# Performance work log

Hardware: AMD Instinct MI355X
Metric: run time of the kernel (lower is better)

Reference implementation:

```python
import jax, jax.numpy as jnp
import numpy as np

N, E, F, K = 50000, 320000, 256, 2

def setup_inputs() -> dict:
    key = jax.random.key(0)
    k0, k1, k2, k3 = jax.random.split(key, 4)
    x = jax.random.normal(k0, (N, F), dtype=jnp.float32)
    edge_index = jax.random.randint(k1, (2, E), 0, N, dtype=jnp.int64)
    s = 1.0 / np.sqrt(F)
    init_weight = jax.random.uniform(k2, (K, F, F), jnp.float32, -s, s)
    root_weight = jax.random.uniform(k3, (K, F, F), jnp.float32, -s, s)
    bias = jnp.zeros((K, 1, F), dtype=jnp.float32)
    return {"x": x, "edge_index": edge_index, "init_weight": init_weight,
            "root_weight": root_weight, "bias": bias}

def reference(x, edge_index, init_weight, root_weight, bias):
    src = edge_index[0]
    dst = edge_index[1]
    n = x.shape[0]
    # gcn_norm without self-loops: deg over target index, sym normalization
    deg = jax.ops.segment_sum(jnp.ones((E,), x.dtype), dst, num_segments=n)
    dinv = jnp.where(deg > 0, jax.lax.rsqrt(jnp.maximum(deg, 1.0)), 0.0)
    w = dinv[src] * dinv[dst]                                   # [E]
    # ARMAConv, num_layers=1: out = act(A_hat @ (x W_k) + x V_k + b_k), mean over K
    h = jnp.einsum('nf,kfg->kng', x, init_weight)               # [K,N,F]
    msg = h[:, src, :] * w[None, :, None]                       # [K,E,F]
    agg = jax.vmap(lambda m: jax.ops.segment_sum(m, dst, num_segments=n))(msg)  # [K,N,F]
    root = jnp.einsum('nf,kfg->kng', x, root_weight)            # [K,N,F]
    arma = jax.nn.relu(agg + root + bias).mean(axis=0)          # [N,F]
    return x + jax.nn.relu(arma)
```

## Files before the change

### kernel.cpp

```cpp
#include <hip/hip_runtime.h>

#define NN 50000
#define NE 320000
#define FF 256
#define FILL_B 1250
#define XCVT_B 12500
#define BPREP_B 128
#define PSTR 64

typedef short short8 __attribute__((ext_vector_type(8)));
typedef float f32x4 __attribute__((ext_vector_type(4)));
typedef unsigned short us4 __attribute__((ext_vector_type(4)));
typedef unsigned short us8 __attribute__((ext_vector_type(8)));

static __device__ __forceinline__ unsigned short f2bf(float f) {
    union { float f; unsigned u; } v; v.f = f;
    unsigned r = v.u + 0x7FFFu + ((v.u >> 16) & 1u);
    return (unsigned short)(r >> 16);
}
static __device__ __forceinline__ float bf2f(unsigned short h) {
    return __uint_as_float((unsigned)h << 16);
}

__global__ __launch_bounds__(256)
void k_pre(const int* __restrict__ ei, int* __restrict__ cnt, int* __restrict__ padded,
           const float* __restrict__ x, unsigned short* __restrict__ Ab,
           const float* __restrict__ wi, const float* __restrict__ wr,
           unsigned short* __restrict__ Bp) {
    const int b = blockIdx.x;
    if (b < FILL_B) {
        int e = b * 256 + threadIdx.x;
        if (e < NE) {
            int src = ei[e];
            int dst = ei[NE + e];
            int slot = atomicAdd(&cnt[dst], 1);
            if (slot < PSTR) padded[(size_t)dst * PSTR + slot] = src;
        }
    } else if (b < FILL_B + XCVT_B) {
        int t = (b - FILL_B) * 256 + threadIdx.x;
        if (t < NN * 64) {
            int n = t >> 6, q = t & 63;
            float4 v = *reinterpret_cast<const float4*>(&x[(size_t)n * FF + q * 4]);
            us4 o = {f2bf(v.x), f2bf(v.y), f2bf(v.z), f2bf(v.w)};
            char* rowp = (char*)(Ab + (size_t)n * 512);
            *reinterpret_cast<us4*>(rowp + ((512 + q * 8) ^ ((n & 7) << 4))) = o;
        }
    } else {
        int t = (b - FILL_B - XCVT_B) * 256 + threadIdx.x;
        int l = t & 63;
        int fb = t >> 6;
        int kc = fb >> 5;
        int cf = fb & 31;
        int col = cf * 16 + (l & 15);
        int kpart = col >> 8;
        int g = col & 255;
        int K0 = kc * 32 + (l >> 4) * 8;
        unsigned short* dst = Bp + (size_t)fb * 512 + (size_t)l * 8;
        #pragma unroll
        for (int e = 0; e < 8; ++e) {
            int K = K0 + e;
            const float* srcp = (K < 256) ? wi : wr;
            float v = srcp[(size_t)kpart * 65536 + (size_t)(K & 255) * 256 + g];
            dst[e] = f2bf(v);
        }
    }
}

__global__ __launch_bounds__(256)
void k_agg(const int* __restrict__ cnt, const int* __restrict__ padded,
           unsigned short* __restrict__ Ab) {
    int wid = (blockIdx.x * blockDim.x + threadIdx.x) >> 6;
    if (wid >= NN / 2) return;
    int l = threadIdx.x & 63;
    int n = wid * 2 + (l >> 5);
    int d = cnt[n];
    float di = d > 0 ? rsqrtf((float)d) : 0.f;
    if (d > PSTR) d = PSTR;
    const int* pp = padded + (size_t)n * PSTR;
    const char* base = (const char*)Ab;
    const int lq = (l & 31) * 16;
    const int lb = 512 + lq;
    float acc[8];
    #pragma unroll
    for (int j = 0; j < 8; ++j) acc[j] = 0.f;
    int e = 0;
    for (; e + 4 <= d; e += 4) {
        int s0 = pp[e + 0];
        int s1 = pp[e + 1];
        int s2 = pp[e + 2];
        int s3 = pp[e + 3];
        us8 v0 = *reinterpret_cast<const us8*>(base + (size_t)s0 * 1024 + (lb ^ ((s0 & 7) << 4)));
        us8 v1 = *reinterpret_cast<const us8*>(base + (size_t)s1 * 1024 + (lb ^ ((s1 & 7) << 4)));
        us8 v2 = *reinterpret_cast<const us8*>(base + (size_t)s2 * 1024 + (lb ^ ((s2 & 7) << 4)));
        us8 v3 = *reinterpret_cast<const us8*>(base + (size_t)s3 * 1024 + (lb ^ ((s3 & 7) << 4)));
        int c0 = cnt[s0], c1 = cnt[s1], c2 = cnt[s2], c3 = cnt[s3];
        float w0 = di * (c0 > 0 ? rsqrtf((float)c0) : 0.f);
        float w1 = di * (c1 > 0 ? rsqrtf((float)c1) : 0.f);
        float w2 = di * (c2 > 0 ? rsqrtf((float)c2) : 0.f);
        float w3 = di * (c3 > 0 ? rsqrtf((float)c3) : 0.f);
        #pragma unroll
        for (int j = 0; j < 8; ++j)
            acc[j] = fmaf(w0, bf2f(v0[j]), fmaf(w1, bf2f(v1[j]),
                     fmaf(w2, bf2f(v2[j]), fmaf(w3, bf2f(v3[j]), acc[j]))));
    }
    for (; e < d; ++e) {
        int s0 = pp[e];
        us8 v0 = *reinterpret_cast<const us8*>(base + (size_t)s0 * 1024 + (lb ^ ((s0 & 7) << 4)));
        int c0 = cnt[s0];
        float w0 = di * (c0 > 0 ? rsqrtf((float)c0) : 0.f);
        #pragma unroll
        for (int j = 0; j < 8; ++j)
            acc[j] = fmaf(w0, bf2f(v0[j]), acc[j]);
    }
    us8 o;
    #pragma unroll
    for (int j = 0; j < 8; ++j) o[j] = f2bf(acc[j]);
    *reinterpret_cast<us8*>((char*)Ab + (size_t)n * 1024 + (lq ^ ((n & 7) << 4))) = o;
}

#define LOADB(dst, kc_)                                                           \
    {                                                                             \
        dst[0] = *reinterpret_cast<const short8*>(bpb + (kc_) * 32768 + (2 * w + 0) * 1024);        \
        dst[1] = *reinterpret_cast<const short8*>(bpb + (kc_) * 32768 + (2 * w + 1) * 1024);        \
        dst[2] = *reinterpret_cast<const short8*>(bpb + (kc_) * 32768 + (16 + 2 * w) * 1024);       \
        dst[3] = *reinterpret_cast<const short8*>(bpb + (kc_) * 32768 + (17 + 2 * w) * 1024);       \
    }
#define LOADA1K(dst, ab, kc2_)                                                    \
    {                                                                             \
        _Pragma("unroll")                                                         \
        for (int rf = 0; rf < 4; ++rf)                                            \
            dst[rf] = *reinterpret_cast<const short8*>((ab) + rf * 16384 + (kc2_) * 128); \
    }
#define MFMA4(aset, bset)                                                         \
    {                                                                             \
        _Pragma("unroll")                                                         \
        for (int rf = 0; rf < 4; ++rf)                                            \
            _Pragma("unroll")                                                     \
            for (int c = 0; c < 4; ++c)                                           \
                acc[rf][c] = __builtin_amdgcn_mfma_f32_16x16x32_bf16(aset[rf], bset[c], acc[rf][c], 0, 0, 0); \
    }

__global__ __launch_bounds__(512, 4)
void k_mm(const unsigned short* __restrict__ Ab, const unsigned short* __restrict__ Bp,
          const float* __restrict__ bias, float* __restrict__ out) {
    __shared__ char smem[65536];

    const int l = threadIdx.x & 63;
    const int w = threadIdx.x >> 6;
    const int row0 = blockIdx.x * 64;

    {
        const char* base = (const char*)Ab;
        #pragma unroll
        for (int j = 0; j < 8; ++j) {
            int rl = j * 8 + w;
            int rsrc = row0 + rl; if (rsrc >= NN) rsrc = NN - 1;
            const char* gp = base + (size_t)rsrc * 1024 + l * 16;
            __builtin_amdgcn_global_load_lds(
                (const __attribute__((address_space(1))) void*)gp,
                (__attribute__((address_space(3))) void*)(smem + rl * 1024),
                16, 0, 0);
        }
    }
    __syncthreads();

    f32x4 acc[4][4];
    #pragma unroll
    for (int i = 0; i < 4; ++i)
        #pragma unroll
        for (int j = 0; j < 4; ++j) acc[i][j] = (f32x4){0.f, 0.f, 0.f, 0.f};

    const int p = l & 7, q = l >> 4;
    const char* abase0 = smem + (l & 15) * 1024 + ((p >> 2) << 6) + ((q ^ (p & 3)) << 4);
    const char* abase1 = smem + (((size_t)(abase0 - smem)) ^ 64);
    const char* bpb = (const char*)(Bp + (size_t)l * 8);

    short8 b0[4], b1[4], a[4];
    LOADB(b0, 0)
    #pragma unroll 1
    for (int kc2 = 0; kc2 < 7; ++kc2) {
        LOADA1K(a, abase0, kc2)
        LOADB(b1, 2 * kc2 + 1)
        MFMA4(a, b0)
        LOADA1K(a, abase1, kc2)
        LOADB(b0, 2 * kc2 + 2)
        MFMA4(a, b1)
    }
    {
        LOADA1K(a, abase0, 7)
        LOADB(b1, 15)
        MFMA4(a, b0)
        LOADA1K(a, abase1, 7)
        MFMA4(a, b1)
    }

    __syncthreads();

    #pragma unroll
    for (int rf = 0; rf < 4; ++rf) {
        const int rl0 = rf * 16 + (l >> 4) * 4;
        #pragma unroll
        for (int j = 0; j < 4; ++j) {
            int rl = rl0 + j;
            int r = row0 + rl;
            if (r >= NN) continue;
            int sw = (rl & 7) << 4;
            #pragma unroll
            for (int c = 0; c < 2; ++c) {
                int gg = w * 32 + c * 16 + (l & 15);
                unsigned short xb =
                    *reinterpret_cast<const unsigned short*>(&smem[rl * 1024 + ((512 + gg * 2) ^ sw)]);
                float xv = bf2f(xb);
                float c0 = acc[rf][c][j] + bias[gg];
                float c1 = acc[rf][c + 2][j] + bias[256 + gg];
                float arma = 0.5f * (fmaxf(c0, 0.f) + fmaxf(c1, 0.f));
                out[(size_t)r * FF + gg] = xv + fmaxf(arma, 0.f);
            }
        }
    }
}

extern "C" void kernel_launch(void* const* d_in, const int* in_sizes, int n_in,
                              void* d_out, int out_size, void* d_ws, size_t ws_size,
                              hipStream_t stream) {
    const float* x    = (const float*)d_in[0];
    const int*   ei   = (const int*)d_in[1];
    const float* wi   = (const float*)d_in[2];
    const float* wr   = (const float*)d_in[3];
    const float* bias = (const float*)d_in[4];
    float* out = (float*)d_out;

    int* cnt    = (int*)d_ws;
    int* padded = cnt + NN;
    unsigned short* Bp = (unsigned short*)(padded + (size_t)NN * PSTR);
    unsigned short* Ab = (unsigned short*)d_out;

    hipMemsetAsync(cnt, 0, NN * sizeof(int), stream);

    k_pre<<<FILL_B + XCVT_B + BPREP_B, 256, 0, stream>>>(ei, cnt, padded, x, Ab, wi, wr, Bp);
    k_agg<<<(NN / 2 * 64 + 255) / 256, 256, 0, stream>>>(cnt, padded, Ab);
    k_mm <<<(NN + 63) / 64, 512, 0, stream>>>(Ab, Bp, bias, out);
}
```

Measured before the change: 108.2 us.

## Split A tile into two K-halves in LDS and start MFMA after first half arrives

```diff
diff --git a/kernel.cpp b/kernel.cpp
--- a/kernel.cpp
+++ b/kernel.cpp
@@ -125,11 +125,11 @@
         dst[2] = *reinterpret_cast<const short8*>(bpb + (kc_) * 32768 + (16 + 2 * w) * 1024);       \
         dst[3] = *reinterpret_cast<const short8*>(bpb + (kc_) * 32768 + (17 + 2 * w) * 1024);       \
     }
-#define LOADA1K(dst, ab, kc2_)                                                    \
+#define LOADAF(dst, ab, h_)                                                       \
     {                                                                             \
         _Pragma("unroll")                                                         \
         for (int rf = 0; rf < 4; ++rf)                                            \
-            dst[rf] = *reinterpret_cast<const short8*>((ab) + rf * 16384 + (kc2_) * 128); \
+            dst[rf] = *reinterpret_cast<const short8*>((ab) + rf * 8192 + (h_) * 128); \
     }
 #define MFMA4(aset, bset)                                                         \
     {                                                                             \
@@ -148,21 +148,30 @@
     const int l = threadIdx.x & 63;
     const int w = threadIdx.x >> 6;
     const int row0 = blockIdx.x * 64;
-
-    {
-        const char* base = (const char*)Ab;
-        #pragma unroll
-        for (int j = 0; j < 8; ++j) {
-            int rl = j * 8 + w;
-            int rsrc = row0 + rl; if (rsrc >= NN) rsrc = NN - 1;
-            const char* gp = base + (size_t)rsrc * 1024 + l * 16;
-            __builtin_amdgcn_global_load_lds(
-                (const __attribute__((address_space(1))) void*)gp,
-                (__attribute__((address_space(3))) void*)(smem + rl * 1024),
-                16, 0, 0);
-        }
-    }
-    __syncthreads();
+    const char* base = (const char*)Ab;
+
+    #pragma unroll
+    for (int j = 0; j < 4; ++j) {
+        int rl = w * 8 + 2 * j;
+        int r = row0 + rl + (l >> 5);
+        if (r >= NN) r = NN - 1;
+        const char* gp = base + (size_t)r * 1024 + (l & 31) * 16;
+        __builtin_amdgcn_global_load_lds(
+            (const __attribute__((address_space(1))) void*)gp,
+            (__attribute__((address_space(3))) void*)(smem + rl * 512),
+            16, 0, 0);
+    }
+    #pragma unroll
+    for (int j = 0; j < 4; ++j) {
+        int rl = w * 8 + 2 * j;
+        int r = row0 + rl + (l >> 5);
+        if (r >= NN) r = NN - 1;
+        const char* gp = base + (size_t)r * 1024 + 512 + (l & 31) * 16;
+        __builtin_amdgcn_global_load_lds(
+            (const __attribute__((address_space(1))) void*)gp,
+            (__attribute__((address_space(3))) void*)(smem + 32768 + rl * 512),
+            16, 0, 0);
+    }
 
     f32x4 acc[4][4];
     #pragma unroll
@@ -171,30 +180,49 @@
         for (int j = 0; j < 4; ++j) acc[i][j] = (f32x4){0.f, 0.f, 0.f, 0.f};
 
     const int p = l & 7, q = l >> 4;
-    const char* abase0 = smem + (l & 15) * 1024 + ((p >> 2) << 6) + ((q ^ (p & 3)) << 4);
-    const char* abase1 = smem + (((size_t)(abase0 - smem)) ^ 64);
+    const int aoff = (l & 15) * 512 + ((p >> 2) << 6) + ((q ^ (p & 3)) << 4);
+    const char* yE = smem + aoff;
+    const char* yO = smem + (aoff ^ 64);
+    const char* xE = smem + 32768 + aoff;
+    const char* xO = smem + 32768 + (aoff ^ 64);
     const char* bpb = (const char*)(Bp + (size_t)l * 8);
 
-    short8 b0[4], b1[4], a[4];
+    short8 a[4], b0[4], b1[4];
     LOADB(b0, 0)
+
+    asm volatile("s_waitcnt vmcnt(8)" ::: "memory");
+    __builtin_amdgcn_s_barrier();
+    __builtin_amdgcn_sched_barrier(0);
+
     #pragma unroll 1
-    for (int kc2 = 0; kc2 < 7; ++kc2) {
-        LOADA1K(a, abase0, kc2)
+    for (int kc2 = 0; kc2 < 4; ++kc2) {
+        LOADAF(a, yE, kc2)
         LOADB(b1, 2 * kc2 + 1)
         MFMA4(a, b0)
-        LOADA1K(a, abase1, kc2)
+        LOADAF(a, yO, kc2)
         LOADB(b0, 2 * kc2 + 2)
         MFMA4(a, b1)
     }
+    asm volatile("s_waitcnt vmcnt(4)" ::: "memory");
+    __builtin_amdgcn_s_barrier();
+    __builtin_amdgcn_sched_barrier(0);
+
+    #pragma unroll 1
+    for (int kc2 = 0; kc2 < 3; ++kc2) {
+        LOADAF(a, xE, kc2)
+        LOADB(b1, 9 + 2 * kc2)
+        MFMA4(a, b0)
+        LOADAF(a, xO, kc2)
+        LOADB(b0, 10 + 2 * kc2)
+        MFMA4(a, b1)
+    }
     {
-        LOADA1K(a, abase0, 7)
+        LOADAF(a, xE, 3)
         LOADB(b1, 15)
         MFMA4(a, b0)
-        LOADA1K(a, abase1, 7)
+        LOADAF(a, xO, 3)
         MFMA4(a, b1)
     }
-
-    __syncthreads();
 
     #pragma unroll
     for (int rf = 0; rf < 4; ++rf) {
@@ -209,7 +237,7 @@
             for (int c = 0; c < 2; ++c) {
                 int gg = w * 32 + c * 16 + (l & 15);
                 unsigned short xb =
-                    *reinterpret_cast<const unsigned short*>(&smem[rl * 1024 + ((512 + gg * 2) ^ sw)]);
+                    *reinterpret_cast<const unsigned short*>(&smem[32768 + rl * 512 + ((gg * 2) ^ sw)]);
                 float xv = bf2f(xb);
                 float c0 = acc[rf][c][j] + bias[gg];
                 float c1 = acc[rf][c + 2][j] + bias[256 + gg];
```

New measurement: 107.7 us. No clear change (-0.5%).
